# Performance work log

Measured on AMD Instinct MI355X. Metric: run time of the kernel, lower is better.

The kernel has to match this reference:

```python
import jax, jax.numpy as jnp
import numpy as np

N_NODES = 100000
N_EDGES = 300000
IN_CH = 256
HID = 256


def setup_inputs() -> dict:
    key = jax.random.key(0)
    k1, k2, k3, k4 = jax.random.split(key, 4)
    z = jax.random.normal(k1, (N_NODES, IN_CH), dtype=jnp.float32)
    edge_index = jax.random.randint(k2, (2, N_EDGES), 0, N_NODES, dtype=jnp.int64)
    # Linear params (torch default init ~ U(-1/sqrt(fan_in), 1/sqrt(fan_in)))
    b1s = 1.0 / np.sqrt(2 * IN_CH)
    b2s = 1.0 / np.sqrt(HID)
    W1 = jax.random.uniform(k3, (HID, 2 * IN_CH), minval=-b1s, maxval=b1s, dtype=jnp.float32)
    b1 = jnp.zeros((HID,), dtype=jnp.float32)
    W2 = jax.random.uniform(k4, (1, HID), minval=-b2s, maxval=b2s, dtype=jnp.float32)
    b2 = jnp.zeros((1,), dtype=jnp.float32)
    return {"z": z, "W1": W1, "b1": b1, "W2": W2, "b2": b2, "edge_index": edge_index}


def reference(z, W1, b1, W2, b2, edge_index):
    # Gather src/dst node embeddings: [E, D] each
    src = z[edge_index[0]]
    dst = z[edge_index[1]]
    # Avoid materializing concat by splitting W1 into src/dst halves:
    # lin1(cat([src,dst])) == src @ W1[:, :D].T + dst @ W1[:, D:].T + b1
    W1s, W1d = W1[:, :IN_CH], W1[:, IN_CH:]
    h = jnp.einsum('ed,hd->eh', src, W1s) + jnp.einsum('ed,hd->eh', dst, W1d) + b1
    h = jax.nn.relu(h)
    out = jnp.einsum('eh,oh->eo', h, W2) + b2  # [E, 1]
    return out[:, 0]
```

## Files before the change

### kernel.cpp

```cpp
#include <hip/hip_runtime.h>


#define NN 100000
#define NE 300000
#define KD 256
#define NO 512

typedef __attribute__((ext_vector_type(8))) short short8;
typedef __attribute__((ext_vector_type(8))) unsigned short ushort8;
typedef __attribute__((ext_vector_type(4))) float f32x4;
typedef __attribute__((ext_vector_type(4))) unsigned int uint4v;

__device__ __forceinline__ unsigned short f2bf(float f) {
  union { float f; unsigned int u; } v; v.f = f;
  unsigned int u = v.u;
  u += 0x7fffu + ((u >> 16) & 1u);
  return (unsigned short)(u >> 16);
}
__device__ __forceinline__ float bf2f(unsigned short h) {
  union { unsigned int u; float f; } v; v.u = ((unsigned int)h) << 16;
  return v.f;
}
__device__ __forceinline__ unsigned int pkbf(float a, float b) {
  unsigned int ua = __float_as_uint(a) + 0x8000u;
  unsigned int ub = __float_as_uint(b) + 0x8000u;
  return __builtin_amdgcn_perm(ub, ua, 0x07060302u);
}

__global__ void prep_w(const float* __restrict__ W1, unsigned short* __restrict__ Wt) {
  int idx = blockIdx.x * 256 + threadIdx.x;
  int j = idx >> 8, k = idx & 255;
  float v = (j < 256) ? W1[j * 512 + k] : W1[(j - 256) * 512 + 256 + k];
  Wt[idx] = f2bf(v);
}

__global__ __launch_bounds__(256, 2) void gemm_zw(const float* __restrict__ z,
                                                  const unsigned short* __restrict__ Wt,
                                                  unsigned short* __restrict__ C) {
  __shared__ unsigned short Bs[128 * KD];

  const int b = blockIdx.x;
  const int xcd = b & 7;
  const int rr = b >> 3;
  const int q = rr & 3;
  const int g = (rr >> 2) * 8 + xcd;
  if (g >= 782) return;
  const int n0 = q * 128;

  const int t = threadIdx.x;
  const int w = t >> 6, lane = t & 63;
  const int l15 = lane & 15, l4 = lane >> 4;

#pragma unroll
  for (int i = 0; i < 16; ++i) {
    const int id = t + 256 * i;
    const int row = id >> 5, c = id & 31;
    ushort8 v = *(const ushort8*)(Wt + (size_t)(n0 + row) * KD + c * 8);
    *(ushort8*)&Bs[row * KD + ((c ^ (row & 7)) << 3)] = v;
  }
  __syncthreads();

  const int slot = g * 4 + w;
  if (slot >= 3125) return;
  const int node0 = slot * 32;

  const float* zr = z + (size_t)(node0 + l15) * KD + l4 * 8;

#define LOADZ(kc, Ra, Rb, Rc, Rd)                                  \
  Ra = *(const float4*)(zr + (kc) * 32);                           \
  Rb = *(const float4*)(zr + (kc) * 32 + 4);                       \
  Rc = *(const float4*)(zr + 16 * KD + (kc) * 32);                 \
  Rd = *(const float4*)(zr + 16 * KD + (kc) * 32 + 4);

  float4 Z0a, Z0b, Z0c, Z0d, Z1a, Z1b, Z1c, Z1d;
  LOADZ(0, Z0a, Z0b, Z0c, Z0d)
  LOADZ(1, Z1a, Z1b, Z1c, Z1d)
  __builtin_amdgcn_sched_barrier(0);

  f32x4 acc0[8], acc1[8];
#pragma unroll
  for (int f = 0; f < 8; ++f) { acc0[f] = (f32x4)0.f; acc1[f] = (f32x4)0.f; }

#define KSTEP(kc, Ra, Rb, Rc, Rd, PF)                                   \
  {                                                                     \
    union { uint4v u; short8 s; } zb0, zb1;                             \
    zb0.u[0] = pkbf(Ra.x, Ra.y); zb0.u[1] = pkbf(Ra.z, Ra.w);           \
    zb0.u[2] = pkbf(Rb.x, Rb.y); zb0.u[3] = pkbf(Rb.z, Rb.w);           \
    zb1.u[0] = pkbf(Rc.x, Rc.y); zb1.u[1] = pkbf(Rc.z, Rc.w);           \
    zb1.u[2] = pkbf(Rd.x, Rd.y); zb1.u[3] = pkbf(Rd.z, Rd.w);           \
    if (PF) { LOADZ((kc) + 2, Ra, Rb, Rc, Rd)                           \
              __builtin_amdgcn_sched_barrier(0); }                      \
    _Pragma("unroll")                                                   \
    for (int f = 0; f < 8; ++f) {                                       \
      union { ushort8 u; short8 s; } wv;                                \
      wv.u = *(const ushort8*)&Bs[(f * 16 + l15) * KD +                 \
                                  ((((kc) * 4 + l4) ^ (l15 & 7)) << 3)];\
      acc0[f] = __builtin_amdgcn_mfma_f32_16x16x32_bf16(wv.s, zb0.s, acc0[f], 0, 0, 0); \
      acc1[f] = __builtin_amdgcn_mfma_f32_16x16x32_bf16(wv.s, zb1.s, acc1[f], 0, 0, 0); \
    }                                                                   \
  }

  KSTEP(0, Z0a, Z0b, Z0c, Z0d, 1)
  KSTEP(1, Z1a, Z1b, Z1c, Z1d, 1)
  KSTEP(2, Z0a, Z0b, Z0c, Z0d, 1)
  KSTEP(3, Z1a, Z1b, Z1c, Z1d, 1)
  KSTEP(4, Z0a, Z0b, Z0c, Z0d, 1)
  KSTEP(5, Z1a, Z1b, Z1c, Z1d, 1)
  KSTEP(6, Z0a, Z0b, Z0c, Z0d, 0)
  KSTEP(7, Z1a, Z1b, Z1c, Z1d, 0)
#undef KSTEP
#undef LOADZ

#pragma unroll
  for (int f = 0; f < 8; ++f) {
    uint2 p;
    p.x = pkbf(acc0[f][0], acc0[f][1]);
    p.y = pkbf(acc0[f][2], acc0[f][3]);
    *(uint2*)(C + (size_t)(node0 + l15) * NO + n0 + f * 16 + l4 * 4) = p;
    p.x = pkbf(acc1[f][0], acc1[f][1]);
    p.y = pkbf(acc1[f][2], acc1[f][3]);
    *(uint2*)(C + (size_t)(node0 + 16 + l15) * NO + n0 + f * 16 + l4 * 4) = p;
  }
}

__global__ __launch_bounds__(256) void edge_mlp(const unsigned short* __restrict__ C,
                                                const int* __restrict__ ei,
                                                const float* __restrict__ b1,
                                                const float* __restrict__ W2,
                                                const float* __restrict__ b2,
                                                float* __restrict__ out) {
  const int t = threadIdx.x;
  const int lane = t & 63;
  const int g = lane >> 4;
  const int c0 = (lane & 15) * 16;
  float b1v[16], w2v[16];
#pragma unroll
  for (int i = 0; i < 16; ++i) { b1v[i] = b1[c0 + i]; w2v[i] = W2[c0 + i]; }
  const float bias2 = b2[0];
  const int waveId = blockIdx.x * 4 + (t >> 6);
  const int nw = gridDim.x * 4;
  for (int e0 = waveId * 4; e0 < NE; e0 += nw * 4) {
    const int e = e0 + g;
    const int sn = ei[e];
    const int dn = ei[NE + e];
    const ushort8* ap = (const ushort8*)(C + (size_t)sn * NO + c0);
    const ushort8* bp = (const ushort8*)(C + (size_t)dn * NO + 256 + c0);
    ushort8 a0 = ap[0], a1 = ap[1];
    ushort8 v0 = bp[0], v1 = bp[1];
    float partial = 0.f;
#pragma unroll
    for (int j = 0; j < 8; ++j) {
      float h = bf2f(a0[j]) + bf2f(v0[j]) + b1v[j];
      h = fmaxf(h, 0.f);
      partial = fmaf(h, w2v[j], partial);
    }
#pragma unroll
    for (int j = 0; j < 8; ++j) {
      float h = bf2f(a1[j]) + bf2f(v1[j]) + b1v[8 + j];
      h = fmaxf(h, 0.f);
      partial = fmaf(h, w2v[8 + j], partial);
    }
    partial += __shfl_xor(partial, 8);
    partial += __shfl_xor(partial, 4);
    partial += __shfl_xor(partial, 2);
    partial += __shfl_xor(partial, 1);
    if ((lane & 15) == 0) out[e] = partial + bias2;
  }
}

extern "C" void kernel_launch(void* const* d_in, const int* in_sizes, int n_in,
                              void* d_out, int out_size, void* d_ws, size_t ws_size,
                              hipStream_t stream) {
  const float* z  = (const float*)d_in[0];
  const float* W1 = (const float*)d_in[1];
  const float* b1 = (const float*)d_in[2];
  const float* W2 = (const float*)d_in[3];
  const float* b2 = (const float*)d_in[4];
  const int*   ei = (const int*)d_in[5];
  float* out = (float*)d_out;

  unsigned short* C  = (unsigned short*)d_ws;
  unsigned short* Wt = C + (size_t)NN * NO;

  prep_w<<<512, 256, 0, stream>>>(W1, Wt);
  gemm_zw<<<3136, 256, 0, stream>>>(z, Wt, C);
  edge_mlp<<<2048, 256, 0, stream>>>(C, ei, b1, W2, b2, out);
}
```

Measured before the change: 126.4 us.

## Process two node tiles per wave to amortize LDS weight staging

Halves the gemm grid so each wave computes two 32-node tiles against the same 128-column weight slice held in shared memory. The 64KB weight staging into LDS is then spread over twice the output. The first z loads for both tiles are now issued before the LDS fill, so global latency overlaps the staging. The cost is a doubled accumulator set, which raises register pressure and risks spills or lower occupancy, plus a tail branch for the last tiles.

Result: slower. 142.1 us (+12.4%).

```diff
diff --git a/kernel.cpp b/kernel.cpp
--- a/kernel.cpp
+++ b/kernel.cpp
@@ -5,6 +5,7 @@
 #define NE 300000
 #define KD 256
 #define NO 512
+#define NBLK 1568
 
 typedef __attribute__((ext_vector_type(8))) short short8;
 typedef __attribute__((ext_vector_type(8))) unsigned short ushort8;
@@ -43,13 +44,37 @@
   const int xcd = b & 7;
   const int rr = b >> 3;
   const int q = rr & 3;
-  const int g = (rr >> 2) * 8 + xcd;
-  if (g >= 782) return;
+  const int gg = (rr >> 2) * 8 + xcd;
   const int n0 = q * 128;
 
   const int t = threadIdx.x;
   const int w = t >> 6, lane = t & 63;
   const int l15 = lane & 15, l4 = lane >> 4;
+
+  const int sigma = gg * 4 + w;
+  const int sA = sigma;
+  const int sB = sigma + NBLK;
+  const bool dual = (sB < 3125);
+
+  const float* zrA = z + (size_t)(sA * 32 + l15) * KD + l4 * 8;
+  const float* zrB = z + (size_t)(sB * 32 + l15) * KD + l4 * 8;
+
+#define LOADZ(ZP, kc, Ra, Rb, Rc, Rd)                              \
+  Ra = *(const float4*)((ZP) + (kc) * 32);                         \
+  Rb = *(const float4*)((ZP) + (kc) * 32 + 4);                     \
+  Rc = *(const float4*)((ZP) + 16 * KD + (kc) * 32);               \
+  Rd = *(const float4*)((ZP) + 16 * KD + (kc) * 32 + 4);
+
+  float4 ZA0a, ZA0b, ZA0c, ZA0d, ZA1a, ZA1b, ZA1c, ZA1d;
+  float4 ZB0a, ZB0b, ZB0c, ZB0d, ZB1a, ZB1b, ZB1c, ZB1d;
+
+  LOADZ(zrA, 0, ZA0a, ZA0b, ZA0c, ZA0d)
+  LOADZ(zrA, 1, ZA1a, ZA1b, ZA1c, ZA1d)
+  if (dual) {
+    LOADZ(zrB, 0, ZB0a, ZB0b, ZB0c, ZB0d)
+    LOADZ(zrB, 1, ZB1a, ZB1b, ZB1c, ZB1d)
+  }
+  __builtin_amdgcn_sched_barrier(0);
 
 #pragma unroll
   for (int i = 0; i < 16; ++i) {
@@ -60,67 +85,72 @@
   }
   __syncthreads();
 
-  const int slot = g * 4 + w;
-  if (slot >= 3125) return;
-  const int node0 = slot * 32;
-
-  const float* zr = z + (size_t)(node0 + l15) * KD + l4 * 8;
-
-#define LOADZ(kc, Ra, Rb, Rc, Rd)                                  \
-  Ra = *(const float4*)(zr + (kc) * 32);                           \
-  Rb = *(const float4*)(zr + (kc) * 32 + 4);                       \
-  Rc = *(const float4*)(zr + 16 * KD + (kc) * 32);                 \
-  Rd = *(const float4*)(zr + 16 * KD + (kc) * 32 + 4);
-
-  float4 Z0a, Z0b, Z0c, Z0d, Z1a, Z1b, Z1c, Z1d;
-  LOADZ(0, Z0a, Z0b, Z0c, Z0d)
-  LOADZ(1, Z1a, Z1b, Z1c, Z1d)
-  __builtin_amdgcn_sched_barrier(0);
-
-  f32x4 acc0[8], acc1[8];
-#pragma unroll
-  for (int f = 0; f < 8; ++f) { acc0[f] = (f32x4)0.f; acc1[f] = (f32x4)0.f; }
-
-#define KSTEP(kc, Ra, Rb, Rc, Rd, PF)                                   \
+  f32x4 accA0[8], accA1[8], accB0[8], accB1[8];
+#pragma unroll
+  for (int f = 0; f < 8; ++f) {
+    accA0[f] = (f32x4)0.f; accA1[f] = (f32x4)0.f;
+    accB0[f] = (f32x4)0.f; accB1[f] = (f32x4)0.f;
+  }
+
+#define PHASE(AC0, AC1, ZP, kc, Ra, Rb, Rc, Rd, PF)                     \
   {                                                                     \
     union { uint4v u; short8 s; } zb0, zb1;                             \
     zb0.u[0] = pkbf(Ra.x, Ra.y); zb0.u[1] = pkbf(Ra.z, Ra.w);           \
     zb0.u[2] = pkbf(Rb.x, Rb.y); zb0.u[3] = pkbf(Rb.z, Rb.w);           \
     zb1.u[0] = pkbf(Rc.x, Rc.y); zb1.u[1] = pkbf(Rc.z, Rc.w);           \
     zb1.u[2] = pkbf(Rd.x, Rd.y); zb1.u[3] = pkbf(Rd.z, Rd.w);           \
-    if (PF) { LOADZ((kc) + 2, Ra, Rb, Rc, Rd)                           \
+    if (PF) { LOADZ(ZP, (kc) + 2, Ra, Rb, Rc, Rd)                       \
               __builtin_amdgcn_sched_barrier(0); }                      \
     _Pragma("unroll")                                                   \
     for (int f = 0; f < 8; ++f) {                                       \
       union { ushort8 u; short8 s; } wv;                                \
       wv.u = *(const ushort8*)&Bs[(f * 16 + l15) * KD +                 \
                                   ((((kc) * 4 + l4) ^ (l15 & 7)) << 3)];\
-      acc0[f] = __builtin_amdgcn_mfma_f32_16x16x32_bf16(wv.s, zb0.s, acc0[f], 0, 0, 0); \
-      acc1[f] = __builtin_amdgcn_mfma_f32_16x16x32_bf16(wv.s, zb1.s, acc1[f], 0, 0, 0); \
+      AC0[f] = __builtin_amdgcn_mfma_f32_16x16x32_bf16(wv.s, zb0.s, AC0[f], 0, 0, 0); \
+      AC1[f] = __builtin_amdgcn_mfma_f32_16x16x32_bf16(wv.s, zb1.s, AC1[f], 0, 0, 0); \
     }                                                                   \
   }
 
-  KSTEP(0, Z0a, Z0b, Z0c, Z0d, 1)
-  KSTEP(1, Z1a, Z1b, Z1c, Z1d, 1)
-  KSTEP(2, Z0a, Z0b, Z0c, Z0d, 1)
-  KSTEP(3, Z1a, Z1b, Z1c, Z1d, 1)
-  KSTEP(4, Z0a, Z0b, Z0c, Z0d, 1)
-  KSTEP(5, Z1a, Z1b, Z1c, Z1d, 1)
-  KSTEP(6, Z0a, Z0b, Z0c, Z0d, 0)
-  KSTEP(7, Z1a, Z1b, Z1c, Z1d, 0)
-#undef KSTEP
+#define PA(kc, Ra, Rb, Rc, Rd, PF) PHASE(accA0, accA1, zrA, kc, Ra, Rb, Rc, Rd, PF)
+#define PB(kc, Ra, Rb, Rc, Rd, PF) PHASE(accB0, accB1, zrB, kc, Ra, Rb, Rc, Rd, PF)
+
+  if (dual) {
+    PA(0, ZA0a, ZA0b, ZA0c, ZA0d, 1) PB(0, ZB0a, ZB0b, ZB0c, ZB0d, 1)
+    PA(1, ZA1a, ZA1b, ZA1c, ZA1d, 1) PB(1, ZB1a, ZB1b, ZB1c, ZB1d, 1)
+    PA(2, ZA0a, ZA0b, ZA0c, ZA0d, 1) PB(2, ZB0a, ZB0b, ZB0c, ZB0d, 1)
+    PA(3, ZA1a, ZA1b, ZA1c, ZA1d, 1) PB(3, ZB1a, ZB1b, ZB1c, ZB1d, 1)
+    PA(4, ZA0a, ZA0b, ZA0c, ZA0d, 1) PB(4, ZB0a, ZB0b, ZB0c, ZB0d, 1)
+    PA(5, ZA1a, ZA1b, ZA1c, ZA1d, 1) PB(5, ZB1a, ZB1b, ZB1c, ZB1d, 1)
+    PA(6, ZA0a, ZA0b, ZA0c, ZA0d, 0) PB(6, ZB0a, ZB0b, ZB0c, ZB0d, 0)
+    PA(7, ZA1a, ZA1b, ZA1c, ZA1d, 0) PB(7, ZB1a, ZB1b, ZB1c, ZB1d, 0)
+  } else {
+    PA(0, ZA0a, ZA0b, ZA0c, ZA0d, 1)
+    PA(1, ZA1a, ZA1b, ZA1c, ZA1d, 1)
+    PA(2, ZA0a, ZA0b, ZA0c, ZA0d, 1)
+    PA(3, ZA1a, ZA1b, ZA1c, ZA1d, 1)
+    PA(4, ZA0a, ZA0b, ZA0c, ZA0d, 1)
+    PA(5, ZA1a, ZA1b, ZA1c, ZA1d, 1)
+    PA(6, ZA0a, ZA0b, ZA0c, ZA0d, 0)
+    PA(7, ZA1a, ZA1b, ZA1c, ZA1d, 0)
+  }
+#undef PA
+#undef PB
+#undef PHASE
 #undef LOADZ
 
-#pragma unroll
-  for (int f = 0; f < 8; ++f) {
-    uint2 p;
-    p.x = pkbf(acc0[f][0], acc0[f][1]);
-    p.y = pkbf(acc0[f][2], acc0[f][3]);
-    *(uint2*)(C + (size_t)(node0 + l15) * NO + n0 + f * 16 + l4 * 4) = p;
-    p.x = pkbf(acc1[f][0], acc1[f][1]);
-    p.y = pkbf(acc1[f][2], acc1[f][3]);
-    *(uint2*)(C + (size_t)(node0 + 16 + l15) * NO + n0 + f * 16 + l4 * 4) = p;
-  }
+#define STOREOUT(node0, A0, A1)                                         \
+  _Pragma("unroll")                                                     \
+  for (int f = 0; f < 8; ++f) {                                         \
+    uint2 p;                                                            \
+    p.x = pkbf(A0[f][0], A0[f][1]); p.y = pkbf(A0[f][2], A0[f][3]);     \
+    *(uint2*)(C + (size_t)((node0) + l15) * NO + n0 + f * 16 + l4 * 4) = p;      \
+    p.x = pkbf(A1[f][0], A1[f][1]); p.y = pkbf(A1[f][2], A1[f][3]);     \
+    *(uint2*)(C + (size_t)((node0) + 16 + l15) * NO + n0 + f * 16 + l4 * 4) = p; \
+  }
+
+  STOREOUT(sA * 32, accA0, accA1)
+  if (dual) { STOREOUT(sB * 32, accB0, accB1) }
+#undef STOREOUT
 }
 
 __global__ __launch_bounds__(256) void edge_mlp(const unsigned short* __restrict__ C,
@@ -183,6 +213,6 @@
   unsigned short* Wt = C + (size_t)NN * NO;
 
   prep_w<<<512, 256, 0, stream>>>(W1, Wt);
-  gemm_zw<<<3136, 256, 0, stream>>>(z, Wt, C);
+  gemm_zw<<<NBLK, 256, 0, stream>>>(z, Wt, C);
   edge_mlp<<<2048, 256, 0, stream>>>(C, ei, b1, W2, b2, out);
 }
```
